# Kernel tuning notes

Measured on AMD Instinct MI355X. Metric: run time of the kernel, lower is better.

## Reference

```python
import jax, jax.numpy as jnp
import numpy as np

OPS = jnp.array([[1,1,1],[1,1,-1],[1,-1,1],[1,-1,-1],[-1,1,1],[-1,1,-1],[-1,-1,1],[-1,-1,-1]], dtype=jnp.float32)  # [8,3] sign flips per eigenvector column

B, N, FN, FE, E = 1, 512, 8, 1, 32
D0 = 6 + FN  # layer-0 node embedding dim: framed (x,v) = 6 dims + node features


def setup_inputs() -> dict:
    key = jax.random.key(0)
    ks = jax.random.split(key, 24)
    rn = lambda k, shp, s=0.1: jax.random.normal(k, shp, jnp.float32) * s
    inp = {
        'node_feat': jax.random.normal(ks[0], (B, N, FN), jnp.float32),
        'edge_feat': jax.random.normal(ks[1], (B, N, N, FE), jnp.float32),
        'x': jax.random.normal(ks[2], (B, N, 3), jnp.float32),
        'v': jax.random.normal(ks[3], (B, N, 3), jnp.float32),
        # GNN layer 0 (input node dim D0)
        'e0_w1': rn(ks[4], (FE + 2 * D0, E)), 'e0_b1': jnp.zeros((E,), jnp.float32),
        'e0_w2': rn(ks[5], (E, E)), 'e0_b2': jnp.zeros((E,), jnp.float32),
        'n0_w1': rn(ks[6], (D0 + E, E)), 'n0_b1': jnp.zeros((E,), jnp.float32),
        'n0_w2': rn(ks[7], (E, E)), 'n0_b2': jnp.zeros((E,), jnp.float32),
        # GNN layer 1 (input node dim E)
        'e1_w1': rn(ks[8], (FE + 2 * E, E)), 'e1_b1': jnp.zeros((E,), jnp.float32),
        'e1_w2': rn(ks[9], (E, E)), 'e1_b2': jnp.zeros((E,), jnp.float32),
        'n1_w1': rn(ks[10], (E + E, E)), 'n1_b1': jnp.zeros((E,), jnp.float32),
        'n1_w2': rn(ks[11], (E, E)), 'n1_b2': jnp.zeros((E,), jnp.float32),
        # decoder: relu -> Linear(E,E) -> relu -> Linear(E,6)
        'dec_w1': rn(ks[12], (E, E)), 'dec_b1': jnp.zeros((E,), jnp.float32),
        'dec_w2': rn(ks[13], (E, 6)), 'dec_b2': jnp.zeros((6,), jnp.float32),
        # v_coef: relu -> Linear(E,E) -> relu -> Linear(E,1)
        'vc_w1': rn(ks[14], (E, E)), 'vc_b1': jnp.zeros((E,), jnp.float32),
        'vc_w2': rn(ks[15], (E, 1)), 'vc_b2': jnp.zeros((1,), jnp.float32),
    }
    return inp


def _gnn_layer(h, edge_feat, ew1, eb1, ew2, eb2, nw1, nb1, nw2, nb2):
    # h: [B,N,d]; edge_feat: [B,N,N,Fe]
    # Torch builds concat([edge_feat, h_j, h_i]) per (i,j) pair; we split W1 rows
    # to avoid materializing the [B,N,N,Fe+2d] concat (same math).
    Fe = edge_feat.shape[-1]
    d = h.shape[-1]
    pre_e = edge_feat @ ew1[:Fe]          # [B,N,N,E]
    pre_j = h @ ew1[Fe:Fe + d]            # [B,N,E], indexed by j
    pre_i = h @ ew1[Fe + d:]              # [B,N,E], indexed by i
    m = jax.nn.relu(pre_e + pre_j[:, None, :, :] + pre_i[:, :, None, :] + eb1)
    m = jax.nn.relu(m @ ew2 + eb2)        # [B,N,N,E]
    agg = m.sum(axis=2)                   # sum over neighbors j -> [B,N,E]
    dn = jax.nn.relu(h @ nw1[:d] + agg @ nw1[d:] + nb1)
    return dn @ nw2 + nb2                 # [B,N,E]


def reference(node_feat, edge_feat, x, v,
              e0_w1, e0_b1, e0_w2, e0_b2, n0_w1, n0_b1, n0_w2, n0_b2,
              e1_w1, e1_b1, e1_w2, e1_b2, n1_w1, n1_b1, n1_w2, n1_b2,
              dec_w1, dec_b1, dec_w2, dec_b2, vc_w1, vc_b1, vc_w2, vc_b2):
    # ---- create_frame (PCA frame averaging) ----
    center = x.mean(axis=1, keepdims=True)                 # [B,1,3]
    xc = x - center
    R = jnp.einsum('bni,bnj->bij', xc, xc)                 # [B,3,3]
    _, Vv = jnp.linalg.eigh(R)                             # eigenvectors, ascending (like torch.symeig)
    F_ops = jax.lax.stop_gradient(OPS[None, :, None, :] * Vv[:, None, :, :])  # [B,8,3,3]
    center = jax.lax.stop_gradient(center)
    xc = x - center
    fx = jnp.einsum('boji,bnj->obni', F_ops, xc)           # [8,B,N,3] (F_ops^T applied)
    fv = jnp.einsum('boji,bnj->obni', F_ops, v)            # [8,B,N,3]
    nf = jnp.broadcast_to(node_feat[None], (8,) + node_feat.shape)
    h0 = jnp.concatenate([fx, fv, nf], axis=-1)            # [8,B,N,6+FN]

    l0 = (e0_w1, e0_b1, e0_w2, e0_b2, n0_w1, n0_b1, n0_w2, n0_b2)
    l1 = (e1_w1, e1_b1, e1_w2, e1_b2, n1_w1, n1_b1, n1_w2, n1_b2)
    frames = []
    for i in range(8):  # small fixed frame count; loop keeps N^2 intermediates per-frame
        hi = _gnn_layer(h0[i], edge_feat, *l0)
        hi = _gnn_layer(hi, edge_feat, *l1)
        frames.append(hi)
    h_out = jnp.stack(frames)                              # [8,B,N,E]

    # ---- decoder + invert_frame ----
    s = jax.nn.relu(jax.nn.relu(h_out) @ dec_w1 + dec_b1)
    spatial_out = s @ dec_w2 + dec_b2                      # [8,B,N,6]
    so = jnp.transpose(spatial_out, (1, 0, 2, 3))          # [B,8,N,6]
    dx = jnp.einsum('boij,bonj->bni', F_ops, so[..., :3]) / 8.0
    dv = jnp.einsum('boij,bonj->bni', F_ops, so[..., 3:]) / 8.0

    h_mean = h_out.mean(axis=0)                            # [B,N,E]
    coef = jax.nn.relu(jax.nn.relu(h_mean) @ vc_w1 + vc_b1) @ vc_w2 + vc_b2  # [B,N,1]
    v_out = v + dv
    x_out = x + v_out * coef + dx
    return (h_mean, edge_feat, x_out, v_out)
```

## Files before the change

kernel.cpp:

```cpp
#include <hip/hip_runtime.h>
#include <hip/hip_bf16.h>
#include <hip/hip_fp16.h>
#include <math.h>

#define NN 512

typedef _Float16 f16x8 __attribute__((ext_vector_type(8)));
typedef float    f32x4 __attribute__((ext_vector_type(4)));

__device__ __forceinline__ void compute_frame(const float* __restrict__ x,
                                              float* __restrict__ sFR,
                                              double (*red)[9]) {
    const int t = threadIdx.x;
    double s[9] = {0,0,0,0,0,0,0,0,0};
    for (int n = t; n < NN; n += 256) {
        double X = x[n*3+0], Y = x[n*3+1], Z = x[n*3+2];
        s[0]+=X; s[1]+=Y; s[2]+=Z;
        s[3]+=X*X; s[4]+=X*Y; s[5]+=X*Z; s[6]+=Y*Y; s[7]+=Y*Z; s[8]+=Z*Z;
    }
    #pragma unroll
    for (int m = 1; m < 64; m <<= 1) {
        #pragma unroll
        for (int q = 0; q < 9; ++q) s[q] += __shfl_xor(s[q], m);
    }
    const int wave = t >> 6, lane = t & 63;
    if (lane == 0) {
        #pragma unroll
        for (int q = 0; q < 9; ++q) red[wave][q] = s[q];
    }
    __syncthreads();
    if (t == 0) {
        double S[9];
        #pragma unroll
        for (int q = 0; q < 9; ++q) S[q] = red[0][q]+red[1][q]+red[2][q]+red[3][q];
        double cx = S[0]/512.0, cy = S[1]/512.0, cz = S[2]/512.0;
        float A[3][3], V[3][3] = {{1,0,0},{0,1,0},{0,0,1}};
        A[0][0]=(float)(S[3]-512.0*cx*cx); A[0][1]=(float)(S[4]-512.0*cx*cy);
        A[0][2]=(float)(S[5]-512.0*cx*cz); A[1][1]=(float)(S[6]-512.0*cy*cy);
        A[1][2]=(float)(S[7]-512.0*cy*cz); A[2][2]=(float)(S[8]-512.0*cz*cz);
        A[1][0]=A[0][1]; A[2][0]=A[0][2]; A[2][1]=A[1][2];
        for (int sweep = 0; sweep < 8; ++sweep) {
            float off = fabsf(A[0][1]) + fabsf(A[0][2]) + fabsf(A[1][2]);
            float dia = fabsf(A[0][0]) + fabsf(A[1][1]) + fabsf(A[2][2]);
            if (off < 1e-7f * (dia + 1e-30f)) break;
            for (int p = 0; p < 3; ++p) for (int q = p+1; q < 3; ++q) {
                float apq = A[p][q];
                if (fabsf(apq) < 1e-30f) continue;
                float tau = (A[q][q] - A[p][p]) / (2.0f * apq);
                float tt = (tau >= 0.f ? 1.0f : -1.0f) / (fabsf(tau) + sqrtf(1.0f + tau*tau));
                float cc = 1.0f / sqrtf(1.0f + tt*tt), ss = tt * cc;
                A[p][p] = A[p][p] - tt * apq;
                A[q][q] = A[q][q] + tt * apq;
                A[p][q] = 0.0f; A[q][p] = 0.0f;
                for (int k = 0; k < 3; ++k) if (k != p && k != q) {
                    float akp = A[k][p], akq = A[k][q];
                    A[k][p] = cc*akp - ss*akq; A[p][k] = A[k][p];
                    A[k][q] = ss*akp + cc*akq; A[q][k] = A[k][q];
                }
                for (int k = 0; k < 3; ++k) {
                    float vkp = V[k][p], vkq = V[k][q];
                    V[k][p] = cc*vkp - ss*vkq;
                    V[k][q] = ss*vkp + cc*vkq;
                }
            }
        }
        float ev[3] = {A[0][0], A[1][1], A[2][2]};
        int idx[3] = {0,1,2};
        for (int a = 0; a < 2; ++a) for (int b = a+1; b < 3; ++b)
            if (ev[idx[b]] < ev[idx[a]]) { int tmp = idx[a]; idx[a] = idx[b]; idx[b] = tmp; }
        sFR[0] = (float)cx; sFR[1] = (float)cy; sFR[2] = (float)cz;
        for (int r = 0; r < 3; ++r)
            for (int c = 0; c < 3; ++c)
                sFR[3 + r*3 + c] = V[r][idx[c]];
    }
    __syncthreads();
}

__global__ void __launch_bounds__(256) pre0_kernel(
    const float* __restrict__ x, const float* __restrict__ v,
    const float* __restrict__ nf,
    const float* __restrict__ e0w1, const float* __restrict__ e0b1,
    const float* __restrict__ e0w2, const float* __restrict__ e1w1,
    const float* __restrict__ e1w2,
    const float* __restrict__ edge,
    float* __restrict__ FRg, float* __restrict__ H0,
    _Float16* __restrict__ PJF, _Float16* __restrict__ PIH,
    _Float16* __restrict__ WEH0, _Float16* __restrict__ WEH1,
    _Float16* __restrict__ W2F0, _Float16* __restrict__ W2F1,
    float* __restrict__ out_edge)
{
    __shared__ double red[4][9];
    __shared__ float sFR[12];
    const int t = threadIdx.x;
    const int b = blockIdx.x;

    ((float2*)out_edge)[b * 256 + t] = ((const float2*)edge)[b * 256 + t];

    compute_frame(x, sFR, red);

    const int lane = t & 63, wv = t >> 6;
    if (b == 0) {
        if (t < 12) FRg[t] = sFR[t];
        const int l15 = lane & 15, kb = (lane >> 4) * 8;
        if (wv == 1) {
            #pragma unroll
            for (int e = 0; e < 8; ++e) {
                W2F0[lane*16 + e]     = (_Float16)e0w2[(kb+e)*32 + l15];
                W2F0[lane*16 + 8 + e] = (_Float16)e0w2[(kb+e)*32 + l15 + 16];
            }
        } else if (wv == 2) {
            #pragma unroll
            for (int e = 0; e < 8; ++e) {
                W2F1[lane*16 + e]     = (_Float16)e1w2[(kb+e)*32 + l15];
                W2F1[lane*16 + 8 + e] = (_Float16)e1w2[(kb+e)*32 + l15 + 16];
            }
        } else if (wv == 3 && lane < 32) {
            WEH0[lane] = (_Float16)e0w1[lane];
            WEH1[lane] = (_Float16)e1w1[lane];
        }
    }

    const int c = t & 31;
    const int row = b * 8 + (t >> 5);
    const int o = row >> 9, j = row & 511;
    float hrow[14];
    float xc0 = x[j*3+0] - sFR[0], xc1 = x[j*3+1] - sFR[1], xc2 = x[j*3+2] - sFR[2];
    float v0 = v[j*3+0], v1 = v[j*3+1], v2 = v[j*3+2];
    #pragma unroll
    for (int i = 0; i < 3; ++i) {
        float sgn = ((o >> (2 - i)) & 1) ? -1.f : 1.f;
        float px = sFR[3 + 0*3 + i]*xc0 + sFR[3 + 1*3 + i]*xc1 + sFR[3 + 2*3 + i]*xc2;
        float pv = sFR[3 + 0*3 + i]*v0  + sFR[3 + 1*3 + i]*v1  + sFR[3 + 2*3 + i]*v2;
        hrow[i]     = sgn * px;
        hrow[3 + i] = sgn * pv;
    }
    #pragma unroll
    for (int k = 0; k < 8; ++k) hrow[6 + k] = nf[j*8 + k];
    if (c < 14) H0[row * 14 + c] = hrow[c];
    float pj = 0.f, pi = e0b1[c];
    #pragma unroll
    for (int k = 0; k < 14; ++k) {
        pj = fmaf(hrow[k], e0w1[(1 + k) * 32 + c], pj);
        pi = fmaf(hrow[k], e0w1[(15 + k) * 32 + c], pi);
    }
    PIH[row * 32 + c] = (_Float16)pi;
    const int fl = (j & 15) | ((c >> 3) << 4);
    PJF[(((o << 5) + (j >> 4)) * 64 + fl) * 8 + (c & 7)] = (_Float16)pj;
}

template<int D, bool NEXT>
__global__ void __launch_bounds__(256, 4) edge_kernel(
    const _Float16* __restrict__ PJF,
    const _Float16* __restrict__ PIH,
    const _Float16* __restrict__ WEH,
    const _Float16* __restrict__ W2F,
    const float* __restrict__ edge,
    const float* __restrict__ h,
    const float* __restrict__ eb2,
    const float* __restrict__ nw1,
    const float* __restrict__ nb1,
    const float* __restrict__ nw2,
    const float* __restrict__ nb2,
    float* __restrict__ hout,
    const float* __restrict__ ew1n,
    const float* __restrict__ eb1n,
    _Float16* __restrict__ PJFn,
    _Float16* __restrict__ PIn)
{
    const int t = threadIdx.x;
    const int wv = t >> 6, lane = t & 63;
    const int o = blockIdx.x >> 8;
    const int i0 = (blockIdx.x & 255) << 1;
    const int i = i0 + (wv & 1);
    const int jh = wv >> 1;
    const int row = (o << 9) | i;
    const int l15 = lane & 15;
    const int kbase = (lane >> 4) * 8;

    __shared__ float sAgg[4][32];

    const f16x8 pi8 = *(const f16x8*)(PIH + row * 32 + kbase);
    const f16x8 we8 = *(const f16x8*)(WEH + kbase);
    const f16x8 bfrag0 = *(const f16x8*)(W2F + lane * 16);
    const f16x8 bfrag1 = *(const f16x8*)(W2F + lane * 16 + 8);
    const float b2v0 = eb2[l15], b2v1 = eb2[l15 + 16];
    const f16x8 z8 = {0,0,0,0,0,0,0,0};
    float agg0 = 0.f, agg1 = 0.f;

    const float* edge_i = edge + (i << 9);
    const _Float16* pjf_o = PJF + (size_t)o * 16384;

    #pragma unroll
    for (int jm = 0; jm < 16; ++jm) {
        const int tile = (jh << 4) | jm;
        const f16x8 pj8 = *(const f16x8*)(pjf_o + (tile * 64 + lane) * 8);
        const _Float16 eh = (_Float16)edge_i[tile * 16 + l15];
        const f16x8 e8 = {eh, eh, eh, eh, eh, eh, eh, eh};
        f16x8 m = e8 * we8 + (pj8 + pi8);
        m = __builtin_elementwise_max(m, z8);
        f32x4 c0 = {0.f, 0.f, 0.f, 0.f};
        c0 = __builtin_amdgcn_mfma_f32_16x16x32_f16(m, bfrag0, c0, 0, 0, 0);
        #pragma unroll
        for (int r = 0; r < 4; ++r) agg0 += fmaxf(c0[r] + b2v0, 0.f);
        f32x4 c1 = {0.f, 0.f, 0.f, 0.f};
        c1 = __builtin_amdgcn_mfma_f32_16x16x32_f16(m, bfrag1, c1, 0, 0, 0);
        #pragma unroll
        for (int r = 0; r < 4; ++r) agg1 += fmaxf(c1[r] + b2v1, 0.f);
    }
    agg0 += __shfl_xor(agg0, 16); agg0 += __shfl_xor(agg0, 32);
    agg1 += __shfl_xor(agg1, 16); agg1 += __shfl_xor(agg1, 32);
    if (lane < 16) { sAgg[wv][l15] = agg0; sAgg[wv][16 + l15] = agg1; }
    __syncthreads();
    if (wv >= 2) return;

    const int c2 = lane & 31;
    const int hf = lane >> 5;
    const int kb = hf << 4;
    const float red2 = sAgg[wv][c2] + sAgg[wv + 2][c2];
    const float* hr = h + row * D;
    constexpr int DH = D / 2;
    float acc = hf ? 0.f : nb1[c2];
    #pragma unroll
    for (int kk = 0; kk < DH; ++kk) {
        const int k = hf * DH + kk;
        acc = fmaf(hr[k], nw1[k * 32 + c2], acc);
    }
    #pragma unroll
    for (int kk = 0; kk < 16; ++kk) {
        const int k = kb + kk;
        acc = fmaf(__shfl(red2, k, 32), nw1[(D + k) * 32 + c2], acc);
    }
    acc += __shfl_xor(acc, 32);
    const float dn = fmaxf(acc, 0.f);
    float outv = hf ? 0.f : nb2[c2];
    #pragma unroll
    for (int kk = 0; kk < 16; ++kk) {
        const int k = kb + kk;
        outv = fmaf(__shfl(dn, k, 32), nw2[k * 32 + c2], outv);
    }
    outv += __shfl_xor(outv, 32);
    if (lane < 32) hout[row * 32 + c2] = outv;

    if (NEXT) {
        float pj1 = 0.f, pi1 = hf ? 0.f : eb1n[c2];
        #pragma unroll
        for (int kk = 0; kk < 16; ++kk) {
            const int k = kb + kk;
            const float hk = __shfl(outv, k, 32);
            pj1 = fmaf(hk, ew1n[(1 + k) * 32 + c2], pj1);
            pi1 = fmaf(hk, ew1n[(33 + k) * 32 + c2], pi1);
        }
        pj1 += __shfl_xor(pj1, 32);
        pi1 += __shfl_xor(pi1, 32);
        if (lane < 32) {
            PIn[row * 32 + c2] = (_Float16)pi1;
            const int fl = (i & 15) | ((c2 >> 3) << 4);
            PJFn[(((o << 5) + (i >> 4)) * 64 + fl) * 8 + (c2 & 7)] = (_Float16)pj1;
        }
    }
}

__global__ void __launch_bounds__(256) decfinal_kernel(
    const float* __restrict__ h2,
    const float* __restrict__ w1, const float* __restrict__ b1,
    const float* __restrict__ w2,
    const float* __restrict__ b2,
    const float* __restrict__ x, const float* __restrict__ v,
    const float* __restrict__ FR,
    const float* __restrict__ vw1, const float* __restrict__ vb1,
    const float* __restrict__ vw2, const float* __restrict__ vb2,
    float* __restrict__ out_hmean, float* __restrict__ out_x,
    float* __restrict__ out_v)
{
    const int n = blockIdx.x;
    const int t = threadIdx.x;
    const int wv = t >> 6, lane = t & 63;
    const int c = lane & 31;
    __shared__ float sSo[8][6];

    #pragma unroll
    for (int q = 0; q < 2; ++q) {
        const int o = (wv << 1) | q;
        const int row = (o << 9) | n;
        float rh = fmaxf(h2[row * 32 + c], 0.f);
        float acc = b1[c];
        #pragma unroll
        for (int k = 0; k < 32; ++k)
            acc = fmaf(__shfl(rh, k, 32), w1[k * 32 + c], acc);
        float s = fmaxf(acc, 0.f);
        #pragma unroll
        for (int m = 0; m < 6; ++m) {
            float p = s * w2[c * 6 + m];
            p += __shfl_xor(p, 1); p += __shfl_xor(p, 2); p += __shfl_xor(p, 4);
            p += __shfl_xor(p, 8); p += __shfl_xor(p, 16);
            if (lane == 0) sSo[o][m] = p + b2[m];
        }
    }
    __syncthreads();
    if (wv) return;

    float hm = 0.f;
    #pragma unroll
    for (int o = 0; o < 8; ++o) hm += h2[((o << 9) | n) * 32 + c];
    hm *= 0.125f;
    if (lane < 32) out_hmean[n * 32 + c] = hm;
    float rh = fmaxf(hm, 0.f);
    float acc = vb1[c];
    #pragma unroll
    for (int k = 0; k < 32; ++k)
        acc = fmaf(__shfl(rh, k, 32), vw1[k * 32 + c], acc);
    float t1 = fmaxf(acc, 0.f);
    float p = t1 * vw2[c];
    p += __shfl_xor(p, 1); p += __shfl_xor(p, 2); p += __shfl_xor(p, 4);
    p += __shfl_xor(p, 8); p += __shfl_xor(p, 16);
    float coef = p + vb2[0];
    if (lane < 3) {
        int i = lane;
        float dx = 0.f, dv = 0.f;
        #pragma unroll
        for (int o = 0; o < 8; ++o) {
            #pragma unroll
            for (int j = 0; j < 3; ++j) {
                float sgn = ((o >> (2 - j)) & 1) ? -1.f : 1.f;
                float f = sgn * FR[3 + i * 3 + j];
                dx = fmaf(f, sSo[o][j], dx);
                dv = fmaf(f, sSo[o][3 + j], dv);
            }
        }
        dx *= 0.125f; dv *= 0.125f;
        float vout = v[n * 3 + i] + dv;
        out_v[n * 3 + i] = vout;
        out_x[n * 3 + i] = x[n * 3 + i] + vout * coef + dx;
    }
}

extern "C" void kernel_launch(void* const* d_in, const int* in_sizes, int n_in,
                              void* d_out, int out_size, void* d_ws, size_t ws_size,
                              hipStream_t stream) {
    const float* node_feat = (const float*)d_in[0];
    const float* edge      = (const float*)d_in[1];
    const float* x         = (const float*)d_in[2];
    const float* v         = (const float*)d_in[3];
    const float* e0_w1 = (const float*)d_in[4];
    const float* e0_b1 = (const float*)d_in[5];
    const float* e0_w2 = (const float*)d_in[6];
    const float* e0_b2 = (const float*)d_in[7];
    const float* n0_w1 = (const float*)d_in[8];
    const float* n0_b1 = (const float*)d_in[9];
    const float* n0_w2 = (const float*)d_in[10];
    const float* n0_b2 = (const float*)d_in[11];
    const float* e1_w1 = (const float*)d_in[12];
    const float* e1_b1 = (const float*)d_in[13];
    const float* e1_w2 = (const float*)d_in[14];
    const float* e1_b2 = (const float*)d_in[15];
    const float* n1_w1 = (const float*)d_in[16];
    const float* n1_b1 = (const float*)d_in[17];
    const float* n1_w2 = (const float*)d_in[18];
    const float* n1_b2 = (const float*)d_in[19];
    const float* dec_w1 = (const float*)d_in[20];
    const float* dec_b1 = (const float*)d_in[21];
    const float* dec_w2 = (const float*)d_in[22];
    const float* dec_b2 = (const float*)d_in[23];
    const float* vc_w1 = (const float*)d_in[24];
    const float* vc_b1 = (const float*)d_in[25];
    const float* vc_w2 = (const float*)d_in[26];
    const float* vc_b2 = (const float*)d_in[27];

    char* wsb = (char*)d_ws;
    float* out = (float*)d_out;

    float*    FR   = (float*)wsb;
    float*    H0   = (float*)(wsb + 256);
    float*    HA   = (float*)(wsb + 256 + 229376);
    float*    HB   = (float*)(wsb + 256 + 229376 + 524288);
    char*     p    = wsb + 256 + 229376 + 524288 + 524288;
    _Float16* PJF0 = (_Float16*)p;            p += 262144;
    _Float16* PIH0 = (_Float16*)p;            p += 262144;
    _Float16* PJF1 = (_Float16*)p;            p += 262144;
    _Float16* PIH1 = (_Float16*)p;            p += 262144;
    _Float16* WEH0 = (_Float16*)p;            p += 256;
    _Float16* WEH1 = (_Float16*)p;            p += 256;
    _Float16* W2F0 = (_Float16*)p;            p += 2048;
    _Float16* W2F1 = (_Float16*)p;            p += 2048;

    pre0_kernel<<<512, 256, 0, stream>>>(x, v, node_feat,
                                         e0_w1, e0_b1, e0_w2, e1_w1, e1_w2,
                                         edge, FR, H0, PJF0, PIH0,
                                         WEH0, WEH1, W2F0, W2F1, out + 16384);
    edge_kernel<14, true><<<2048, 256, 0, stream>>>(
        PJF0, PIH0, WEH0, W2F0, edge, H0, e0_b2, n0_w1, n0_b1, n0_w2, n0_b2,
        HA, e1_w1, e1_b1, PJF1, PIH1);
    edge_kernel<32, false><<<2048, 256, 0, stream>>>(
        PJF1, PIH1, WEH1, W2F1, edge, HA, e1_b2, n1_w1, n1_b1, n1_w2, n1_b2,
        HB, nullptr, nullptr, nullptr, nullptr);
    decfinal_kernel<<<512, 256, 0, stream>>>(HB, dec_w1, dec_b1, dec_w2, dec_b2,
                                             x, v, FR, vc_w1, vc_b1, vc_w2, vc_b2,
                                             out, out + 278528, out + 280064);
}
```

Before: 156.0 us.

## Fuse decoder into layer-1 edge kernel and remap blocks to node-per-block

Each block now handles one destination node i across all 8 frames, with each wave processing two frames over all 512 source tiles. This replaces the earlier scheme of 2 nodes by 1 frame per block with the j range split across waves. Edge features for row i are loaded once per wave and shared by the two frames, and no shared-memory reduction between waves is needed. The decoder and final invert/v_coef stage now run inside the layer-1 edge kernel, which drops one launch and the HB round trip through global memory. The trade-offs are fewer blocks (512 instead of 2048), a launch_bounds occupancy hint of 2, and longer per-wave serial loops.

```diff
diff --git a/kernel.cpp b/kernel.cpp
--- a/kernel.cpp
+++ b/kernel.cpp
@@ -148,75 +148,17 @@
     PJF[(((o << 5) + (j >> 4)) * 64 + fl) * 8 + (c & 7)] = (_Float16)pj;
 }
 
-template<int D, bool NEXT>
-__global__ void __launch_bounds__(256, 4) edge_kernel(
-    const _Float16* __restrict__ PJF,
-    const _Float16* __restrict__ PIH,
-    const _Float16* __restrict__ WEH,
-    const _Float16* __restrict__ W2F,
-    const float* __restrict__ edge,
+template<int D>
+__device__ __forceinline__ float node_mlp(
+    const int row, const float red2,
     const float* __restrict__ h,
-    const float* __restrict__ eb2,
-    const float* __restrict__ nw1,
-    const float* __restrict__ nb1,
-    const float* __restrict__ nw2,
-    const float* __restrict__ nb2,
-    float* __restrict__ hout,
-    const float* __restrict__ ew1n,
-    const float* __restrict__ eb1n,
-    _Float16* __restrict__ PJFn,
-    _Float16* __restrict__ PIn)
+    const float* __restrict__ nw1, const float* __restrict__ nb1,
+    const float* __restrict__ nw2, const float* __restrict__ nb2)
 {
-    const int t = threadIdx.x;
-    const int wv = t >> 6, lane = t & 63;
-    const int o = blockIdx.x >> 8;
-    const int i0 = (blockIdx.x & 255) << 1;
-    const int i = i0 + (wv & 1);
-    const int jh = wv >> 1;
-    const int row = (o << 9) | i;
-    const int l15 = lane & 15;
-    const int kbase = (lane >> 4) * 8;
-
-    __shared__ float sAgg[4][32];
-
-    const f16x8 pi8 = *(const f16x8*)(PIH + row * 32 + kbase);
-    const f16x8 we8 = *(const f16x8*)(WEH + kbase);
-    const f16x8 bfrag0 = *(const f16x8*)(W2F + lane * 16);
-    const f16x8 bfrag1 = *(const f16x8*)(W2F + lane * 16 + 8);
-    const float b2v0 = eb2[l15], b2v1 = eb2[l15 + 16];
-    const f16x8 z8 = {0,0,0,0,0,0,0,0};
-    float agg0 = 0.f, agg1 = 0.f;
-
-    const float* edge_i = edge + (i << 9);
-    const _Float16* pjf_o = PJF + (size_t)o * 16384;
-
-    #pragma unroll
-    for (int jm = 0; jm < 16; ++jm) {
-        const int tile = (jh << 4) | jm;
-        const f16x8 pj8 = *(const f16x8*)(pjf_o + (tile * 64 + lane) * 8);
-        const _Float16 eh = (_Float16)edge_i[tile * 16 + l15];
-        const f16x8 e8 = {eh, eh, eh, eh, eh, eh, eh, eh};
-        f16x8 m = e8 * we8 + (pj8 + pi8);
-        m = __builtin_elementwise_max(m, z8);
-        f32x4 c0 = {0.f, 0.f, 0.f, 0.f};
-        c0 = __builtin_amdgcn_mfma_f32_16x16x32_f16(m, bfrag0, c0, 0, 0, 0);
-        #pragma unroll
-        for (int r = 0; r < 4; ++r) agg0 += fmaxf(c0[r] + b2v0, 0.f);
-        f32x4 c1 = {0.f, 0.f, 0.f, 0.f};
-        c1 = __builtin_amdgcn_mfma_f32_16x16x32_f16(m, bfrag1, c1, 0, 0, 0);
-        #pragma unroll
-        for (int r = 0; r < 4; ++r) agg1 += fmaxf(c1[r] + b2v1, 0.f);
-    }
-    agg0 += __shfl_xor(agg0, 16); agg0 += __shfl_xor(agg0, 32);
-    agg1 += __shfl_xor(agg1, 16); agg1 += __shfl_xor(agg1, 32);
-    if (lane < 16) { sAgg[wv][l15] = agg0; sAgg[wv][16 + l15] = agg1; }
-    __syncthreads();
-    if (wv >= 2) return;
-
+    const int lane = threadIdx.x & 63;
     const int c2 = lane & 31;
     const int hf = lane >> 5;
     const int kb = hf << 4;
-    const float red2 = sAgg[wv][c2] + sAgg[wv + 2][c2];
     const float* hr = h + row * D;
     constexpr int DH = D / 2;
     float acc = hf ? 0.f : nb1[c2];
@@ -239,9 +181,97 @@
         outv = fmaf(__shfl(dn, k, 32), nw2[k * 32 + c2], outv);
     }
     outv += __shfl_xor(outv, 32);
-    if (lane < 32) hout[row * 32 + c2] = outv;
-
-    if (NEXT) {
+    return outv;
+}
+
+__device__ __forceinline__ void edge_pair(
+    const int o0, const int i,
+    const _Float16* __restrict__ PJF, const _Float16* __restrict__ PIH,
+    const _Float16* __restrict__ WEH, const _Float16* __restrict__ W2F,
+    const float* __restrict__ edge, const float* __restrict__ eb2,
+    float& redA, float& redB)
+{
+    const int lane = threadIdx.x & 63;
+    const int l15 = lane & 15;
+    const int kbase = (lane >> 4) * 8;
+    const int rowA = (o0 << 9) | i;
+
+    const f16x8 piA = *(const f16x8*)(PIH + rowA * 32 + kbase);
+    const f16x8 piB = *(const f16x8*)(PIH + (rowA + 512) * 32 + kbase);
+    const f16x8 we8 = *(const f16x8*)(WEH + kbase);
+    const f16x8 bf0 = *(const f16x8*)(W2F + lane * 16);
+    const f16x8 bf1 = *(const f16x8*)(W2F + lane * 16 + 8);
+    const float b2v0 = eb2[l15], b2v1 = eb2[l15 + 16];
+    const f16x8 z8 = {0,0,0,0,0,0,0,0};
+    float aggA0 = 0.f, aggA1 = 0.f, aggB0 = 0.f, aggB1 = 0.f;
+
+    const float* edge_i = edge + (i << 9);
+    const _Float16* pjfA = PJF + (size_t)o0 * 16384;
+    const _Float16* pjfB = pjfA + 16384;
+
+    #pragma unroll 4
+    for (int tile = 0; tile < 32; ++tile) {
+        const _Float16 eh = (_Float16)edge_i[tile * 16 + l15];
+        const f16x8 e8 = {eh, eh, eh, eh, eh, eh, eh, eh};
+        const f16x8 pjA = *(const f16x8*)(pjfA + (tile * 64 + lane) * 8);
+        const f16x8 pjB = *(const f16x8*)(pjfB + (tile * 64 + lane) * 8);
+        f16x8 mA = e8 * we8 + (pjA + piA);
+        mA = __builtin_elementwise_max(mA, z8);
+        f16x8 mB = e8 * we8 + (pjB + piB);
+        mB = __builtin_elementwise_max(mB, z8);
+        f32x4 c;
+        c = (f32x4){0.f,0.f,0.f,0.f};
+        c = __builtin_amdgcn_mfma_f32_16x16x32_f16(mA, bf0, c, 0, 0, 0);
+        #pragma unroll
+        for (int r = 0; r < 4; ++r) aggA0 += fmaxf(c[r] + b2v0, 0.f);
+        c = (f32x4){0.f,0.f,0.f,0.f};
+        c = __builtin_amdgcn_mfma_f32_16x16x32_f16(mA, bf1, c, 0, 0, 0);
+        #pragma unroll
+        for (int r = 0; r < 4; ++r) aggA1 += fmaxf(c[r] + b2v1, 0.f);
+        c = (f32x4){0.f,0.f,0.f,0.f};
+        c = __builtin_amdgcn_mfma_f32_16x16x32_f16(mB, bf0, c, 0, 0, 0);
+        #pragma unroll
+        for (int r = 0; r < 4; ++r) aggB0 += fmaxf(c[r] + b2v0, 0.f);
+        c = (f32x4){0.f,0.f,0.f,0.f};
+        c = __builtin_amdgcn_mfma_f32_16x16x32_f16(mB, bf1, c, 0, 0, 0);
+        #pragma unroll
+        for (int r = 0; r < 4; ++r) aggB1 += fmaxf(c[r] + b2v1, 0.f);
+    }
+    aggA0 += __shfl_xor(aggA0, 16); aggA0 += __shfl_xor(aggA0, 32);
+    aggA1 += __shfl_xor(aggA1, 16); aggA1 += __shfl_xor(aggA1, 32);
+    aggB0 += __shfl_xor(aggB0, 16); aggB0 += __shfl_xor(aggB0, 32);
+    aggB1 += __shfl_xor(aggB1, 16); aggB1 += __shfl_xor(aggB1, 32);
+    redA = (lane & 16) ? aggA1 : aggA0;
+    redB = (lane & 16) ? aggB1 : aggB0;
+}
+
+__global__ void __launch_bounds__(256, 2) edgeA_kernel(
+    const _Float16* __restrict__ PJF, const _Float16* __restrict__ PIH,
+    const _Float16* __restrict__ WEH, const _Float16* __restrict__ W2F,
+    const float* __restrict__ edge, const float* __restrict__ h,
+    const float* __restrict__ eb2,
+    const float* __restrict__ nw1, const float* __restrict__ nb1,
+    const float* __restrict__ nw2, const float* __restrict__ nb2,
+    float* __restrict__ hout,
+    const float* __restrict__ ew1n, const float* __restrict__ eb1n,
+    _Float16* __restrict__ PJFn, _Float16* __restrict__ PIn)
+{
+    const int i = blockIdx.x;
+    const int wv = threadIdx.x >> 6, lane = threadIdx.x & 63;
+    const int o0 = wv << 1;
+    float redA, redB;
+    edge_pair(o0, i, PJF, PIH, WEH, W2F, edge, eb2, redA, redB);
+
+    const int c2 = lane & 31;
+    const int hf = lane >> 5;
+    const int kb = hf << 4;
+    const int fl = (i & 15) | ((c2 >> 3) << 4);
+    #pragma unroll
+    for (int q = 0; q < 2; ++q) {
+        const int o = o0 + q;
+        const int row = (o << 9) | i;
+        const float outv = node_mlp<14>(row, q ? redB : redA, h, nw1, nb1, nw2, nb2);
+        if (lane < 32) hout[row * 32 + c2] = outv;
         float pj1 = 0.f, pi1 = hf ? 0.f : eb1n[c2];
         #pragma unroll
         for (int kk = 0; kk < 16; ++kk) {
@@ -254,17 +284,20 @@
         pi1 += __shfl_xor(pi1, 32);
         if (lane < 32) {
             PIn[row * 32 + c2] = (_Float16)pi1;
-            const int fl = (i & 15) | ((c2 >> 3) << 4);
             PJFn[(((o << 5) + (i >> 4)) * 64 + fl) * 8 + (c2 & 7)] = (_Float16)pj1;
         }
     }
 }
 
-__global__ void __launch_bounds__(256) decfinal_kernel(
-    const float* __restrict__ h2,
-    const float* __restrict__ w1, const float* __restrict__ b1,
-    const float* __restrict__ w2,
-    const float* __restrict__ b2,
+__global__ void __launch_bounds__(256, 2) edgeB_kernel(
+    const _Float16* __restrict__ PJF, const _Float16* __restrict__ PIH,
+    const _Float16* __restrict__ WEH, const _Float16* __restrict__ W2F,
+    const float* __restrict__ edge, const float* __restrict__ h,
+    const float* __restrict__ eb2,
+    const float* __restrict__ nw1, const float* __restrict__ nb1,
+    const float* __restrict__ nw2, const float* __restrict__ nb2,
+    const float* __restrict__ dw1, const float* __restrict__ db1,
+    const float* __restrict__ dw2, const float* __restrict__ db2,
     const float* __restrict__ x, const float* __restrict__ v,
     const float* __restrict__ FR,
     const float* __restrict__ vw1, const float* __restrict__ vb1,
@@ -272,65 +305,70 @@
     float* __restrict__ out_hmean, float* __restrict__ out_x,
     float* __restrict__ out_v)
 {
-    const int n = blockIdx.x;
-    const int t = threadIdx.x;
-    const int wv = t >> 6, lane = t & 63;
+    const int i = blockIdx.x;
+    const int wv = threadIdx.x >> 6, lane = threadIdx.x & 63;
+    const int o0 = wv << 1;
+    __shared__ float sSo[8][6];
+    __shared__ float sHM[4][32];
+
+    float redA, redB;
+    edge_pair(o0, i, PJF, PIH, WEH, W2F, edge, eb2, redA, redB);
+
+    const float outA = node_mlp<32>((o0 << 9) | i, redA, h, nw1, nb1, nw2, nb2);
+    const float outB = node_mlp<32>(((o0 + 1) << 9) | i, redB, h, nw1, nb1, nw2, nb2);
+
     const int c = lane & 31;
-    __shared__ float sSo[8][6];
+    if (lane < 32) sHM[wv][c] = outA + outB;
 
     #pragma unroll
     for (int q = 0; q < 2; ++q) {
-        const int o = (wv << 1) | q;
-        const int row = (o << 9) | n;
-        float rh = fmaxf(h2[row * 32 + c], 0.f);
-        float acc = b1[c];
+        const int o = o0 + q;
+        const float rh = fmaxf(q ? outB : outA, 0.f);
+        float acc = db1[c];
         #pragma unroll
         for (int k = 0; k < 32; ++k)
-            acc = fmaf(__shfl(rh, k, 32), w1[k * 32 + c], acc);
-        float s = fmaxf(acc, 0.f);
+            acc = fmaf(__shfl(rh, k, 32), dw1[k * 32 + c], acc);
+        const float s = fmaxf(acc, 0.f);
         #pragma unroll
         for (int m = 0; m < 6; ++m) {
-            float p = s * w2[c * 6 + m];
+            float p = s * dw2[c * 6 + m];
             p += __shfl_xor(p, 1); p += __shfl_xor(p, 2); p += __shfl_xor(p, 4);
             p += __shfl_xor(p, 8); p += __shfl_xor(p, 16);
-            if (lane == 0) sSo[o][m] = p + b2[m];
+            if (lane == 0) sSo[o][m] = p + db2[m];
         }
     }
     __syncthreads();
     if (wv) return;
 
-    float hm = 0.f;
-    #pragma unroll
-    for (int o = 0; o < 8; ++o) hm += h2[((o << 9) | n) * 32 + c];
-    hm *= 0.125f;
-    if (lane < 32) out_hmean[n * 32 + c] = hm;
-    float rh = fmaxf(hm, 0.f);
+    const float hm = (sHM[0][c] + sHM[1][c] + sHM[2][c] + sHM[3][c]) * 0.125f;
+    if (lane < 32) out_hmean[i * 32 + c] = hm;
+    const float rh = fmaxf(hm, 0.f);
     float acc = vb1[c];
     #pragma unroll
     for (int k = 0; k < 32; ++k)
         acc = fmaf(__shfl(rh, k, 32), vw1[k * 32 + c], acc);
-    float t1 = fmaxf(acc, 0.f);
+    const float t1 = fmaxf(acc, 0.f);
     float p = t1 * vw2[c];
     p += __shfl_xor(p, 1); p += __shfl_xor(p, 2); p += __shfl_xor(p, 4);
     p += __shfl_xor(p, 8); p += __shfl_xor(p, 16);
-    float coef = p + vb2[0];
+    const float coef = p + vb2[0];
     if (lane < 3) {
-        int i = lane;
+        const int ii = lane;
         float dx = 0.f, dv = 0.f;
         #pragma unroll
         for (int o = 0; o < 8; ++o) {
             #pragma unroll
             for (int j = 0; j < 3; ++j) {
                 float sgn = ((o >> (2 - j)) & 1) ? -1.f : 1.f;
-                float f = sgn * FR[3 + i * 3 + j];
+                float f = sgn * FR[3 + ii * 3 + j];
                 dx = fmaf(f, sSo[o][j], dx);
                 dv = fmaf(f, sSo[o][3 + j], dv);
             }
         }
         dx *= 0.125f; dv *= 0.125f;
-        float vout = v[n * 3 + i] + dv;
-        out_v[n * 3 + i] = vout;
-        out_x[n * 3 + i] = x[n * 3 + i] + vout * coef + dx;
+        const float vout = v[i * 3 + ii] + dv;
+        out_v[i * 3 + ii] = vout;
+        out_x[i * 3 + ii] = x[i * 3 + ii] + vout * coef + dx;
     }
 }
 
@@ -372,7 +410,6 @@
     float*    FR   = (float*)wsb;
     float*    H0   = (float*)(wsb + 256);
     float*    HA   = (float*)(wsb + 256 + 229376);
-    float*    HB   = (float*)(wsb + 256 + 229376 + 524288);
     char*     p    = wsb + 256 + 229376 + 524288 + 524288;
     _Float16* PJF0 = (_Float16*)p;            p += 262144;
     _Float16* PIH0 = (_Float16*)p;            p += 262144;
@@ -387,13 +424,12 @@
                                          e0_w1, e0_b1, e0_w2, e1_w1, e1_w2,
                                          edge, FR, H0, PJF0, PIH0,
                                          WEH0, WEH1, W2F0, W2F1, out + 16384);
-    edge_kernel<14, true><<<2048, 256, 0, stream>>>(
+    edgeA_kernel<<<512, 256, 0, stream>>>(
         PJF0, PIH0, WEH0, W2F0, edge, H0, e0_b2, n0_w1, n0_b1, n0_w2, n0_b2,
         HA, e1_w1, e1_b1, PJF1, PIH1);
-    edge_kernel<32, false><<<2048, 256, 0, stream>>>(
+    edgeB_kernel<<<512, 256, 0, stream>>>(
         PJF1, PIH1, WEH1, W2F1, edge, HA, e1_b2, n1_w1, n1_b1, n1_w2, n1_b2,
-        HB, nullptr, nullptr, nullptr, nullptr);
-    decfinal_kernel<<<512, 256, 0, stream>>>(HB, dec_w1, dec_b1, dec_w2, dec_b2,
-                                             x, v, FR, vc_w1, vc_b1, vc_w2, vc_b2,
-                                             out, out + 278528, out + 280064);
-}
+        dec_w1, dec_b1, dec_w2, dec_b2, x, v, FR,
+        vc_w1, vc_b1, vc_w2, vc_b2,
+        out, out + 278528, out + 280064);
+}
```

Result: no change. 155.5 us (median of 2 runs) (-0.3%).

## Assign one full edge row per wave and drop shared-memory reduction

Applied to the files above, without the earlier changes.

Each wave now processes all 32 j-tiles for a single (frame, i) row instead of splitting the j range across two waves. This removes the shared-memory partial-sum exchange, the block barrier and the idle half-block during the node MLP, since every wave runs its own node update. The grid is halved to keep one wave per row. The trade-off is twice the serial loop length per wave and half as many resident waves to hide load latency.

```diff
diff --git a/kernel.cpp b/kernel.cpp
--- a/kernel.cpp
+++ b/kernel.cpp
@@ -167,22 +167,18 @@
     _Float16* __restrict__ PJFn,
     _Float16* __restrict__ PIn)
 {
-    const int t = threadIdx.x;
-    const int wv = t >> 6, lane = t & 63;
-    const int o = blockIdx.x >> 8;
-    const int i0 = (blockIdx.x & 255) << 1;
-    const int i = i0 + (wv & 1);
-    const int jh = wv >> 1;
-    const int row = (o << 9) | i;
+    const int lane = threadIdx.x & 63;
+    const int w = (blockIdx.x << 2) | (threadIdx.x >> 6);
+    const int o = w >> 9;
+    const int i = w & 511;
+    const int row = w;
     const int l15 = lane & 15;
     const int kbase = (lane >> 4) * 8;
 
-    __shared__ float sAgg[4][32];
-
     const f16x8 pi8 = *(const f16x8*)(PIH + row * 32 + kbase);
     const f16x8 we8 = *(const f16x8*)(WEH + kbase);
-    const f16x8 bfrag0 = *(const f16x8*)(W2F + lane * 16);
-    const f16x8 bfrag1 = *(const f16x8*)(W2F + lane * 16 + 8);
+    const f16x8 bf0 = *(const f16x8*)(W2F + lane * 16);
+    const f16x8 bf1 = *(const f16x8*)(W2F + lane * 16 + 8);
     const float b2v0 = eb2[l15], b2v1 = eb2[l15 + 16];
     const f16x8 z8 = {0,0,0,0,0,0,0,0};
     float agg0 = 0.f, agg1 = 0.f;
@@ -190,33 +186,29 @@
     const float* edge_i = edge + (i << 9);
     const _Float16* pjf_o = PJF + (size_t)o * 16384;
 
-    #pragma unroll
-    for (int jm = 0; jm < 16; ++jm) {
-        const int tile = (jh << 4) | jm;
+    #pragma unroll 8
+    for (int tile = 0; tile < 32; ++tile) {
         const f16x8 pj8 = *(const f16x8*)(pjf_o + (tile * 64 + lane) * 8);
         const _Float16 eh = (_Float16)edge_i[tile * 16 + l15];
         const f16x8 e8 = {eh, eh, eh, eh, eh, eh, eh, eh};
         f16x8 m = e8 * we8 + (pj8 + pi8);
         m = __builtin_elementwise_max(m, z8);
         f32x4 c0 = {0.f, 0.f, 0.f, 0.f};
-        c0 = __builtin_amdgcn_mfma_f32_16x16x32_f16(m, bfrag0, c0, 0, 0, 0);
+        c0 = __builtin_amdgcn_mfma_f32_16x16x32_f16(m, bf0, c0, 0, 0, 0);
         #pragma unroll
         for (int r = 0; r < 4; ++r) agg0 += fmaxf(c0[r] + b2v0, 0.f);
         f32x4 c1 = {0.f, 0.f, 0.f, 0.f};
-        c1 = __builtin_amdgcn_mfma_f32_16x16x32_f16(m, bfrag1, c1, 0, 0, 0);
+        c1 = __builtin_amdgcn_mfma_f32_16x16x32_f16(m, bf1, c1, 0, 0, 0);
         #pragma unroll
         for (int r = 0; r < 4; ++r) agg1 += fmaxf(c1[r] + b2v1, 0.f);
     }
     agg0 += __shfl_xor(agg0, 16); agg0 += __shfl_xor(agg0, 32);
     agg1 += __shfl_xor(agg1, 16); agg1 += __shfl_xor(agg1, 32);
-    if (lane < 16) { sAgg[wv][l15] = agg0; sAgg[wv][16 + l15] = agg1; }
-    __syncthreads();
-    if (wv >= 2) return;
+    const float red2 = (lane & 16) ? agg1 : agg0;
 
     const int c2 = lane & 31;
     const int hf = lane >> 5;
     const int kb = hf << 4;
-    const float red2 = sAgg[wv][c2] + sAgg[wv + 2][c2];
     const float* hr = h + row * D;
     constexpr int DH = D / 2;
     float acc = hf ? 0.f : nb1[c2];
@@ -387,10 +379,10 @@
                                          e0_w1, e0_b1, e0_w2, e1_w1, e1_w2,
                                          edge, FR, H0, PJF0, PIH0,
                                          WEH0, WEH1, W2F0, W2F1, out + 16384);
-    edge_kernel<14, true><<<2048, 256, 0, stream>>>(
+    edge_kernel<14, true><<<1024, 256, 0, stream>>>(
         PJF0, PIH0, WEH0, W2F0, edge, H0, e0_b2, n0_w1, n0_b1, n0_w2, n0_b2,
         HA, e1_w1, e1_b1, PJF1, PIH1);
-    edge_kernel<32, false><<<2048, 256, 0, stream>>>(
+    edge_kernel<32, false><<<1024, 256, 0, stream>>>(
         PJF1, PIH1, WEH1, W2F1, edge, HA, e1_b2, n1_w1, n1_b1, n1_w2, n1_b2,
         HB, nullptr, nullptr, nullptr, nullptr);
     decfinal_kernel<<<512, 256, 0, stream>>>(HB, dec_w1, dec_b1, dec_w2, dec_b2,
```

Result: no change. 158.6 us (+1.6%).
